# Kernel tuning notes

Measured on AMD Instinct MI355X. Metric: run time of the kernel, lower is better.

The kernel has to match this reference:

```python
import jax, jax.numpy as jnp
import numpy as np

NUM_HEADS = 8
SPARSITY = 0.25
BOUNDARY_W = 0.5
LN_EPS = 1e-5


def setup_inputs() -> dict:
    key = jax.random.key(0)
    ks = jax.random.split(key, 16)
    B, C, H, W = 8, 256, 64, 64
    Ch = C // 4
    s = lambda *sh: 1.0 / np.sqrt(sh[-1])
    inp = {
        'x': jax.random.normal(ks[0], (B, C, H, W), jnp.float32),
        'boundary_map': jax.random.uniform(ks[1], (B, 1, H, W), jnp.float32),
        'imp_w1': jax.random.normal(ks[2], (Ch, C), jnp.float32) * s(C),
        'imp_b1': jnp.zeros((Ch,), jnp.float32),
        'imp_w2': jax.random.normal(ks[3], (1, Ch), jnp.float32) * s(Ch),
        'imp_b2': jnp.zeros((1,), jnp.float32),
        'wq': jax.random.normal(ks[4], (C, C), jnp.float32) * s(C),
        'bq': jnp.zeros((C,), jnp.float32),
        'wk': jax.random.normal(ks[5], (C, C), jnp.float32) * s(C),
        'bk': jnp.zeros((C,), jnp.float32),
        'wv': jax.random.normal(ks[6], (C, C), jnp.float32) * s(C),
        'bv': jnp.zeros((C,), jnp.float32),
        'wo': jax.random.normal(ks[7], (C, C), jnp.float32) * (0.1 * s(C)),
        'bo': jnp.zeros((C,), jnp.float32),
        'ln_g': jnp.ones((C,), jnp.float32),
        'ln_b': jnp.zeros((C,), jnp.float32),
    }
    return inp


def reference(x, boundary_map, imp_w1, imp_b1, imp_w2, imp_b2,
              wq, bq, wk, bk, wv, bv, wo, bo, ln_g, ln_b):
    B, C, H, W = x.shape
    N = H * W
    K = max(int(N * SPARSITY), 1)
    nh = NUM_HEADS
    hd = C // nh
    scale = hd ** -0.5

    # importance net: 1x1 conv -> GELU -> 1x1 conv -> sigmoid
    h = jnp.einsum('bchw,oc->bohw', x, imp_w1) + imp_b1[None, :, None, None]
    h = jax.nn.gelu(h, approximate=False)
    imp = jnp.einsum('bchw,oc->bohw', h, imp_w2) + imp_b2[None, :, None, None]
    importance = jax.nn.sigmoid(imp) + BOUNDARY_W * boundary_map  # [B,1,H,W]

    # top-K token selection
    _, top_idx = jax.lax.top_k(importance.reshape(B, N), K)  # [B,K]

    x_flat = x.transpose(0, 2, 3, 1).reshape(B, N, C)
    x_sp = jnp.take_along_axis(x_flat, top_idx[..., None], axis=1)  # [B,K,C]

    # sparse self-attention over K tokens
    q = (jnp.einsum('bkc,oc->bko', x_sp, wq) + bq).reshape(B, K, nh, hd)
    k = (jnp.einsum('bkc,oc->bko', x_sp, wk) + bk).reshape(B, K, nh, hd)
    v = (jnp.einsum('bkc,oc->bko', x_sp, wv) + bv).reshape(B, K, nh, hd)
    attn = jax.nn.softmax(jnp.einsum('bqhd,bkhd->bhqk', q, k) * scale, axis=-1)
    o = jnp.einsum('bhqk,bkhd->bqhd', attn, v).reshape(B, K, C)
    out_sp = jnp.einsum('bkc,oc->bko', o, wo) + bo

    # residual + LayerNorm
    y = out_sp + x_sp
    mu = jnp.mean(y, axis=-1, keepdims=True)
    var = jnp.mean(jnp.square(y - mu), axis=-1, keepdims=True)
    enh = (y - mu) * jax.lax.rsqrt(var + LN_EPS) * ln_g + ln_b  # [B,K,C]

    # scatter enhanced tokens back
    bidx = jnp.arange(B)[:, None]
    out_full = x_flat.at[bidx, top_idx].set(enh)
    out = out_full.reshape(B, H, W, C).transpose(0, 3, 1, 2)
    return out, importance
```

## Files before the change

### kernel.cpp

```cpp
#include <hip/hip_runtime.h>
#include <math.h>

#define B_ 8
#define C_ 256
#define N_ 4096
#define K_ 1024
#define NH_ 8
#define HD_ 32

typedef __attribute__((ext_vector_type(8))) short short8;
typedef __attribute__((ext_vector_type(8))) _Float16 half8;
typedef __attribute__((ext_vector_type(4))) _Float16 half4;
typedef __attribute__((ext_vector_type(4))) float f32x4;

#if __has_builtin(__builtin_amdgcn_exp2f)
#define EXPX(x) __builtin_amdgcn_exp2f(x)
#define QSCALE (0.17677669529663688f * 1.4426950408889634f)
#else
#define EXPX(x) __expf(x)
#define QSCALE 0.17677669529663688f
#endif

__device__ __forceinline__ unsigned bfr(float x){
  unsigned u = __float_as_uint(x);
  return (u + 0x7FFFu + ((u >> 16) & 1u)) >> 16;
}
__device__ __forceinline__ unsigned pk2(float lo, float hi){
  return bfr(lo) | (bfr(hi) << 16);
}
__device__ __forceinline__ unsigned hpk(float a, float b){
  _Float16 ha = (_Float16)a, hb = (_Float16)b;
  unsigned short ua = __builtin_bit_cast(unsigned short, ha);
  unsigned short ub = __builtin_bit_cast(unsigned short, hb);
  return (unsigned)ua | ((unsigned)ub << 16);
}
__device__ __forceinline__ half4 pk4rtz(float a, float b, float c, float d){
  auto lo = __builtin_amdgcn_cvt_pkrtz(a, b);
  auto hi = __builtin_amdgcn_cvt_pkrtz(c, d);
  uint2 u = make_uint2(__builtin_bit_cast(unsigned, lo), __builtin_bit_cast(unsigned, hi));
  return __builtin_bit_cast(half4, u);
}

__global__ __launch_bounds__(256) void w2h_kernel(
    const float* __restrict__ wq, const float* __restrict__ wk,
    const float* __restrict__ wv, const float* __restrict__ wo,
    unsigned short* __restrict__ wh)
{
  const float* src = blockIdx.y==0 ? wq : blockIdx.y==1 ? wk : blockIdx.y==2 ? wv : wo;
  const int e = (blockIdx.x*256 + threadIdx.x)*8;
  float4 a = *(const float4*)(src + e);
  float4 b = *(const float4*)(src + e + 4);
  uint4 o;
  o.x = hpk(a.x, a.y); o.y = hpk(a.z, a.w);
  o.z = hpk(b.x, b.y); o.w = hpk(b.z, b.w);
  *(uint4*)(wh + (size_t)blockIdx.y*65536 + e) = o;
}

__global__ __launch_bounds__(256) void imp_kernel(
    const float* __restrict__ x, const float* __restrict__ bmap,
    const float* __restrict__ w1, const float* __restrict__ b1,
    const float* __restrict__ w2, const float* __restrict__ b2,
    float* __restrict__ imp_out, float* __restrict__ outx)
{
  __shared__ float xs[256][32];
  __shared__ float red[4][32];
  const int t = threadIdx.x;
  const int b = blockIdx.x >> 7, tile = blockIdx.x & 127;
  const int n0 = tile * 32;
  {
    const int p4 = t & 7, co = t >> 3;
    const float* xb = x + (size_t)b*C_*N_ + n0 + 4*p4;
    float* ox = outx + (size_t)b*C_*N_ + n0 + 4*p4;
    #pragma unroll
    for (int s = 0; s < 8; s++){
      const int c = s*32 + co;
      float4 v = *(const float4*)(xb + (size_t)c*N_);
      *(float4*)(ox + (size_t)c*N_) = v;
      *(float4*)&xs[c][4*(p4 ^ (c & 7))] = v;
    }
  }
  __syncthreads();
  const int pg = t & 7, og = t >> 3;
  float acc[4][2];
  #pragma unroll
  for (int pp=0;pp<4;pp++){ acc[pp][0]=0.f; acc[pp][1]=0.f; }
  #pragma unroll 2
  for (int c8 = 0; c8 < 256; c8 += 8){
    float4 xv[8];
    #pragma unroll
    for (int ci = 0; ci < 8; ci++){
      const int c = c8 + ci;
      xv[ci] = *(const float4*)&xs[c][4*(pg ^ (c & 7))];
    }
    #pragma unroll
    for (int oo = 0; oo < 2; oo++){
      const float* wr = w1 + (size_t)(og + 32*oo)*C_ + c8;
      float4 wa = *(const float4*)wr;
      float4 wb = *(const float4*)(wr+4);
      #pragma unroll
      for (int pp = 0; pp < 4; pp++){
        const float x0 = (&xv[0].x)[pp], x1 = (&xv[1].x)[pp];
        const float x2 = (&xv[2].x)[pp], x3 = (&xv[3].x)[pp];
        const float x4 = (&xv[4].x)[pp], x5 = (&xv[5].x)[pp];
        const float x6 = (&xv[6].x)[pp], x7 = (&xv[7].x)[pp];
        acc[pp][oo] += x0*wa.x + x1*wa.y + x2*wa.z + x3*wa.w
                     + x4*wb.x + x5*wb.y + x6*wb.z + x7*wb.w;
      }
    }
  }
  float part[4] = {0.f,0.f,0.f,0.f};
  #pragma unroll
  for (int oo=0;oo<2;oo++){
    const int o = og + 32*oo;
    const float b1o = b1[o], w2o = w2[o];
    #pragma unroll
    for (int pp=0;pp<4;pp++){
      float a = acc[pp][oo] + b1o;
      float g = 0.5f*a*(1.f + erff(a*0.70710678118654752f));
      part[pp] += w2o*g;
    }
  }
  #pragma unroll
  for (int pp=0;pp<4;pp++){
    part[pp] += __shfl_xor(part[pp], 8);
    part[pp] += __shfl_xor(part[pp], 16);
    part[pp] += __shfl_xor(part[pp], 32);
  }
  const int w = t >> 6;
  if ((t & 63) < 8){
    #pragma unroll
    for (int pp=0;pp<4;pp++) red[w][4*(t&7)+pp] = part[pp];
  }
  __syncthreads();
  if (t < 32){
    float s = red[0][t]+red[1][t]+red[2][t]+red[3][t] + b2[0];
    float sig = 1.f/(1.f+expf(-s));
    imp_out[(size_t)b*N_ + n0 + t] = sig + 0.5f*bmap[(size_t)b*N_ + n0 + t];
  }
}

__global__ __launch_bounds__(1024) void topk_kernel(const float* __restrict__ imp, int* __restrict__ tidx)
{
  __shared__ unsigned long long s[4096];
  __shared__ int ws2[16];
  const int b = blockIdx.x, t = threadIdx.x;
  const float* ib = imp + (size_t)b*N_;
  for (int m = t; m < N_; m += 1024){
    unsigned u = __float_as_uint(ib[m]);
    u = (u & 0x80000000u) ? ~u : (u | 0x80000000u);
    s[m] = ((unsigned long long)u << 32) | (unsigned)(~m);
  }
  for (int k = 2; k <= 4096; k <<= 1){
    for (int j = k >> 1; j > 0; j >>= 1){
      __syncthreads();
      #pragma unroll 2
      for (int m = t; m < 2048; m += 1024){
        int i = 2*m - (m & (j-1));
        int l = i + j;
        unsigned long long a = s[i], c = s[l];
        if ((a > c) == ((i & k) == 0)){ s[i] = c; s[l] = a; }
      }
    }
  }
  __syncthreads();
  const unsigned long long thr = s[3072];
  int sel[4]; int cnt = 0;
  #pragma unroll
  for (int u2 = 0; u2 < 4; u2++){
    const int m = 4*t + u2;
    unsigned u = __float_as_uint(ib[m]);
    u = (u & 0x80000000u) ? ~u : (u | 0x80000000u);
    unsigned long long key = ((unsigned long long)u << 32) | (unsigned)(~m);
    sel[u2] = (key >= thr) ? 1 : 0;
    cnt += sel[u2];
  }
  int incl = cnt;
  #pragma unroll
  for (int d2 = 1; d2 < 64; d2 <<= 1){
    int v2 = __shfl_up(incl, d2);
    if ((t & 63) >= d2) incl += v2;
  }
  if ((t & 63) == 63) ws2[t >> 6] = incl;
  __syncthreads();
  int base = 0;
  const int wv2 = t >> 6;
  #pragma unroll
  for (int ww = 0; ww < 16; ww++) if (ww < wv2) base += ws2[ww];
  int pos = base + incl - cnt;
  #pragma unroll
  for (int u2 = 0; u2 < 4; u2++){
    if (sel[u2]) tidx[(size_t)b*K_ + pos++] = 4*t + u2;
  }
}

__global__ __launch_bounds__(512) void qkv_kernel(
    const float* __restrict__ x, const int* __restrict__ tidx,
    const unsigned short* __restrict__ wh,
    const float* __restrict__ bq, const float* __restrict__ bk, const float* __restrict__ bv,
    float* __restrict__ xsp, unsigned short* __restrict__ qbf,
    unsigned short* __restrict__ kbf, unsigned short* __restrict__ vtb)
{
  __shared__ unsigned short xsb[16][256];
  const int t = threadIdx.x;
  const int kt = blockIdx.x, b = blockIdx.y;
  const int tok0 = kt*16;
  {
    const int i = t & 15, jg = t >> 4;
    const int n = tidx[(size_t)b*K_ + tok0 + i];
    const float* xb = x + (size_t)b*C_*N_ + n;
    float v[8];
    #pragma unroll
    for (int u = 0; u < 8; u++) v[u] = xb[(size_t)(jg*8+u)*N_];
    float* xr = xsp + ((size_t)b*K_ + tok0 + i)*C_ + jg*8;
    *(float4*)(xr)     = make_float4(v[0],v[1],v[2],v[3]);
    *(float4*)(xr + 4) = make_float4(v[4],v[5],v[6],v[7]);
    uint4 pw;
    pw.x = hpk(v[0],v[1]); pw.y = hpk(v[2],v[3]);
    pw.z = hpk(v[4],v[5]); pw.w = hpk(v[6],v[7]);
    *(uint4*)((char*)&xsb[0][0] + i*512 + ((jg ^ (i&7))*16)) = pw;
  }
  __syncthreads();

  const int lane = t & 63, w = t >> 6;
  const int g = lane >> 4, c = lane & 15;

  f32x4 acc[3][2];
  #pragma unroll
  for (int s=0;s<3;s++)
    #pragma unroll
    for (int j=0;j<2;j++) acc[s][j] = (f32x4){0.f,0.f,0.f,0.f};

  #pragma unroll 1
  for (int ks = 0; ks < 8; ks++){
    half8 Xf = *(const half8*)((const char*)&xsb[0][0] + c*512 + (((4*ks+g) ^ (c&7))*16));
    half8 Wf[3][2];
    #pragma unroll
    for (int s=0;s<3;s++)
      #pragma unroll
      for (int j=0;j<2;j++)
        Wf[s][j] = *(const half8*)(wh + (size_t)s*65536 + (32*w + 16*j + c)*C_ + ks*32 + 8*g);
    acc[0][0] = __builtin_amdgcn_mfma_f32_16x16x32_f16(Wf[0][0], Xf, acc[0][0], 0,0,0);
    acc[0][1] = __builtin_amdgcn_mfma_f32_16x16x32_f16(Wf[0][1], Xf, acc[0][1], 0,0,0);
    acc[1][0] = __builtin_amdgcn_mfma_f32_16x16x32_f16(Wf[1][0], Xf, acc[1][0], 0,0,0);
    acc[1][1] = __builtin_amdgcn_mfma_f32_16x16x32_f16(Wf[1][1], Xf, acc[1][1], 0,0,0);
    acc[2][0] = __builtin_amdgcn_mfma_f32_16x16x32_f16(Xf, Wf[2][0], acc[2][0], 0,0,0);
    acc[2][1] = __builtin_amdgcn_mfma_f32_16x16x32_f16(Xf, Wf[2][1], acc[2][1], 0,0,0);
  }

  const int bh = b*NH_ + w;
  #pragma unroll
  for (int s=0;s<2;s++){
    const float* bias = s ? bk : bq;
    const float sc = s ? 1.f : QSCALE;
    unsigned short* dstb = s ? kbf : qbf;
    #pragma unroll
    for (int j=0;j<2;j++){
      f32x4 a = acc[s][j];
      float4 bb = *(const float4*)(bias + w*32 + 16*j + 4*g);
      unsigned lo = pk2((a[0]+bb.x)*sc, (a[1]+bb.y)*sc);
      unsigned hi = pk2((a[2]+bb.z)*sc, (a[3]+bb.w)*sc);
      unsigned short* dst = dstb + ((size_t)bh*K_ + tok0 + c)*HD_ + 16*j + 4*g;
      *(uint2*)dst = make_uint2(lo, hi);
    }
  }
  const int base32 = tok0 & ~31;
  const int half   = (tok0 >> 4) & 1;
  #pragma unroll
  for (int j=0;j<2;j++){
    f32x4 a = acc[2][j];
    const float bvv = bv[w*32 + 16*j + c];
    unsigned lo = hpk(a[0]+bvv, a[1]+bvv);
    unsigned hi = hpk(a[2]+bvv, a[3]+bvv);
    unsigned short* dst = vtb + ((size_t)bh*HD_ + 16*j + c)*K_ + base32 + 8*g + 4*half;
    *(uint2*)dst = make_uint2(lo, hi);
  }
}

__global__ __launch_bounds__(512) void attn_kernel(
    const unsigned short* __restrict__ qbf, const unsigned short* __restrict__ kbf,
    const unsigned short* __restrict__ vtb, unsigned short* __restrict__ ob)
{
  __shared__ float po[4][64][19];
  const int tid = threadIdx.x;
  const int t = tid & 63, w = tid >> 6;
  const int sp = w >> 2, qq = w & 3;
  const int flat = blockIdx.x;
  const int h = flat & 7;
  const int rest = flat >> 3;
  const int qt = rest & 7;
  const int b = rest >> 3;
  const int g = t >> 4, c = t & 15;
  const int bh = b*NH_ + h;
  const int q0 = qt*128 + qq*32;

  short8 Qf0 = *(const short8*)(qbf + ((size_t)bh*K_ + q0 + c)*HD_ + g*8);
  short8 Qf1 = *(const short8*)(qbf + ((size_t)bh*K_ + q0 + 16 + c)*HD_ + g*8);

  const int kbeg = sp*512;
  const unsigned short* kp  = kbf + (size_t)bh*K_*HD_ + (size_t)(kbeg + c)*HD_ + g*8;
  const unsigned short* vp0 = vtb + ((size_t)bh*HD_ + c)*K_ + kbeg + g*8;
  const unsigned short* vp1 = vp0 + (size_t)16*K_;

  const half4 ONES = {(_Float16)1.f, (_Float16)1.f, (_Float16)1.f, (_Float16)1.f};
  f32x4 ot00 = {0.f,0.f,0.f,0.f}, ot01 = {0.f,0.f,0.f,0.f};
  f32x4 ot10 = {0.f,0.f,0.f,0.f}, ot11 = {0.f,0.f,0.f,0.f};
  f32x4 otL0 = {0.f,0.f,0.f,0.f}, otL1 = {0.f,0.f,0.f,0.f};

#define ATTN_STEP(K0c,K1c,V0c,V1c) do {                                           \
    f32x4 z = {0.f,0.f,0.f,0.f};                                                  \
    __builtin_amdgcn_s_setprio(1);                                                \
    f32x4 s00 = __builtin_amdgcn_mfma_f32_16x16x32_bf16(K0c, Qf0, z, 0, 0, 0);    \
    f32x4 s01 = __builtin_amdgcn_mfma_f32_16x16x32_bf16(K1c, Qf0, z, 0, 0, 0);    \
    f32x4 s10 = __builtin_amdgcn_mfma_f32_16x16x32_bf16(K0c, Qf1, z, 0, 0, 0);    \
    f32x4 s11 = __builtin_amdgcn_mfma_f32_16x16x32_bf16(K1c, Qf1, z, 0, 0, 0);    \
    __builtin_amdgcn_s_setprio(0);                                                \
    float p00[4], p01[4], p10[4], p11[4];                                         \
    _Pragma("unroll")                                                             \
    for (int r=0;r<4;r++){                                                        \
      p00[r] = EXPX(s00[r]); p01[r] = EXPX(s01[r]);                               \
      p10[r] = EXPX(s10[r]); p11[r] = EXPX(s11[r]);                               \
    }                                                                             \
    half4 P00 = pk4rtz(p00[0], p00[1], p00[2], p00[3]);                           \
    half4 P01 = pk4rtz(p01[0], p01[1], p01[2], p01[3]);                           \
    half4 P10 = pk4rtz(p10[0], p10[1], p10[2], p10[3]);                           \
    half4 P11 = pk4rtz(p11[0], p11[1], p11[2], p11[3]);                           \
    half4 A0lo = __builtin_shufflevector(V0c, V0c, 0, 1, 2, 3);                   \
    half4 A0hi = __builtin_shufflevector(V0c, V0c, 4, 5, 6, 7);                   \
    half4 A1lo = __builtin_shufflevector(V1c, V1c, 0, 1, 2, 3);                   \
    half4 A1hi = __builtin_shufflevector(V1c, V1c, 4, 5, 6, 7);                   \
    __builtin_amdgcn_s_setprio(1);                                                \
    ot00 = __builtin_amdgcn_mfma_f32_16x16x16f16(A0lo, P00, ot00, 0, 0, 0);       \
    ot00 = __builtin_amdgcn_mfma_f32_16x16x16f16(A0hi, P01, ot00, 0, 0, 0);       \
    ot01 = __builtin_amdgcn_mfma_f32_16x16x16f16(A1lo, P00, ot01, 0, 0, 0);       \
    ot01 = __builtin_amdgcn_mfma_f32_16x16x16f16(A1hi, P01, ot01, 0, 0, 0);       \
    ot10 = __builtin_amdgcn_mfma_f32_16x16x16f16(A0lo, P10, ot10, 0, 0, 0);       \
    ot10 = __builtin_amdgcn_mfma_f32_16x16x16f16(A0hi, P11, ot10, 0, 0, 0);       \
    ot11 = __builtin_amdgcn_mfma_f32_16x16x16f16(A1lo, P10, ot11, 0, 0, 0);       \
    ot11 = __builtin_amdgcn_mfma_f32_16x16x16f16(A1hi, P11, ot11, 0, 0, 0);       \
    otL0 = __builtin_amdgcn_mfma_f32_16x16x16f16(ONES, P00, otL0, 0, 0, 0);       \
    otL0 = __builtin_amdgcn_mfma_f32_16x16x16f16(ONES, P01, otL0, 0, 0, 0);       \
    otL1 = __builtin_amdgcn_mfma_f32_16x16x16f16(ONES, P10, otL1, 0, 0, 0);       \
    otL1 = __builtin_amdgcn_mfma_f32_16x16x16f16(ONES, P11, otL1, 0, 0, 0);       \
    __builtin_amdgcn_s_setprio(0);                                                \
  } while(0)

  short8 K0a = *(const short8*)(kp);
  short8 K1a = *(const short8*)(kp + 16*HD_);
  half8  V0a = *(const half8*)(vp0);
  half8  V1a = *(const half8*)(vp1);
  kp += 32*HD_; vp0 += 32; vp1 += 32;
  short8 K0b = *(const short8*)(kp);
  short8 K1b = *(const short8*)(kp + 16*HD_);
  half8  V0b = *(const half8*)(vp0);
  half8  V1b = *(const half8*)(vp1);

  for (int it = 0; it < 16; it += 2){
    kp += 32*HD_; vp0 += 32; vp1 += 32;
    short8 K0n = *(const short8*)(kp);
    short8 K1n = *(const short8*)(kp + 16*HD_);
    half8  V0n = *(const half8*)(vp0);
    half8  V1n = *(const half8*)(vp1);
    ATTN_STEP(K0a, K1a, V0a, V1a);
    K0a = K0n; K1a = K1n; V0a = V0n; V1a = V1n;
    kp += 32*HD_; vp0 += 32; vp1 += 32;
    short8 K0m = *(const short8*)(kp);
    short8 K1m = *(const short8*)(kp + 16*HD_);
    half8  V0m = *(const half8*)(vp0);
    half8  V1m = *(const half8*)(vp1);
    ATTN_STEP(K0b, K1b, V0b, V1b);
    K0b = K0m; K1b = K1m; V0b = V0m; V1b = V1m;
  }
#undef ATTN_STEP

  if (sp == 1){
    float* d = po[qq][t];
    d[0]=ot00[0]; d[1]=ot00[1]; d[2]=ot00[2];  d[3]=ot00[3];
    d[4]=ot01[0]; d[5]=ot01[1]; d[6]=ot01[2];  d[7]=ot01[3];
    d[8]=ot10[0]; d[9]=ot10[1]; d[10]=ot10[2]; d[11]=ot10[3];
    d[12]=ot11[0];d[13]=ot11[1];d[14]=ot11[2]; d[15]=ot11[3];
    d[16]=otL0[0]; d[17]=otL1[0];
  }
  __syncthreads();
  if (sp == 0){
    const float* d = po[qq][t];
    ot00[0]+=d[0]; ot00[1]+=d[1]; ot00[2]+=d[2];  ot00[3]+=d[3];
    ot01[0]+=d[4]; ot01[1]+=d[5]; ot01[2]+=d[6];  ot01[3]+=d[7];
    ot10[0]+=d[8]; ot10[1]+=d[9]; ot10[2]+=d[10]; ot10[3]+=d[11];
    ot11[0]+=d[12];ot11[1]+=d[13];ot11[2]+=d[14]; ot11[3]+=d[15];
    const float L0 = otL0[0] + d[16];
    const float L1 = otL1[0] + d[17];
    const float i0 = 1.f / L0, i1 = 1.f / L1;
    unsigned short* o0 = ob + ((size_t)b*K_ + q0 + c)*C_ + h*HD_;
    unsigned short* o1 = ob + ((size_t)b*K_ + q0 + 16 + c)*C_ + h*HD_;
    *(uint2*)(o0 + 4*g)      = make_uint2(hpk(ot00[0]*i0, ot00[1]*i0), hpk(ot00[2]*i0, ot00[3]*i0));
    *(uint2*)(o0 + 16 + 4*g) = make_uint2(hpk(ot01[0]*i0, ot01[1]*i0), hpk(ot01[2]*i0, ot01[3]*i0));
    *(uint2*)(o1 + 4*g)      = make_uint2(hpk(ot10[0]*i1, ot10[1]*i1), hpk(ot10[2]*i1, ot10[3]*i1));
    *(uint2*)(o1 + 16 + 4*g) = make_uint2(hpk(ot11[0]*i1, ot11[1]*i1), hpk(ot11[2]*i1, ot11[3]*i1));
  }
}

__global__ __launch_bounds__(512) void out_kernel(
    const unsigned short* __restrict__ ob, const float* __restrict__ xsp,
    const int* __restrict__ tidx, const unsigned short* __restrict__ woh, const float* __restrict__ bo,
    const float* __restrict__ lng, const float* __restrict__ lnb,
    float* __restrict__ out)
{
  __shared__ float red1[8][32], red2[8][32];
  __shared__ float mus[32], rss[32];
  __shared__ int nn[32];
  const int t = threadIdx.x;
  const int kt = blockIdx.x, b = blockIdx.y;
  const int tok0 = kt*32;
  const int lane = t & 63, w = t >> 6;
  const int g = lane >> 4, c = lane & 15;

  if (t < 32) nn[t] = tidx[(size_t)b*K_ + tok0 + t];

  f32x4 acc[2][2];
  #pragma unroll
  for (int j=0;j<2;j++)
    #pragma unroll
    for (int tt=0;tt<2;tt++) acc[j][tt] = (f32x4){0.f,0.f,0.f,0.f};

  const unsigned short* ob0 = ob + ((size_t)b*K_ + tok0)*C_;
  const unsigned short* wr0 = woh + (32*w + c)*C_;

  #pragma unroll 1
  for (int ks = 0; ks < 8; ks++){
    half8 Wf0 = *(const half8*)(wr0 + ks*32 + 8*g);
    half8 Wf1 = *(const half8*)(wr0 + 16*C_ + ks*32 + 8*g);
    #pragma unroll
    for (int tt=0;tt<2;tt++){
      half8 Of = *(const half8*)(ob0 + (size_t)(16*tt + c)*C_ + ks*32 + 8*g);
      acc[0][tt] = __builtin_amdgcn_mfma_f32_16x16x32_f16(Wf0, Of, acc[0][tt], 0,0,0);
      acc[1][tt] = __builtin_amdgcn_mfma_f32_16x16x32_f16(Wf1, Of, acc[1][tt], 0,0,0);
    }
  }

  float4 bb[2];
  #pragma unroll
  for (int j=0;j<2;j++) bb[j] = *(const float4*)(bo + 32*w + 16*j + 4*g);
  #pragma unroll
  for (int tt=0;tt<2;tt++){
    const float* xr = xsp + ((size_t)b*K_ + tok0 + 16*tt + c)*C_ + 32*w + 4*g;
    #pragma unroll
    for (int j=0;j<2;j++){
      float4 xv = *(const float4*)(xr + 16*j);
      acc[j][tt][0] += bb[j].x + xv.x;
      acc[j][tt][1] += bb[j].y + xv.y;
      acc[j][tt][2] += bb[j].z + xv.z;
      acc[j][tt][3] += bb[j].w + xv.w;
    }
  }

  #pragma unroll
  for (int tt=0;tt<2;tt++){
    float s1 = 0.f, s2 = 0.f;
    #pragma unroll
    for (int j=0;j<2;j++)
      #pragma unroll
      for (int r=0;r<4;r++){ float y = acc[j][tt][r]; s1 += y; s2 += y*y; }
    s1 += __shfl_xor(s1, 16); s2 += __shfl_xor(s2, 16);
    s1 += __shfl_xor(s1, 32); s2 += __shfl_xor(s2, 32);
    if (g == 0){ red1[w][16*tt + c] = s1; red2[w][16*tt + c] = s2; }
  }
  __syncthreads();
  if (t < 32){
    float a = 0.f, q2 = 0.f;
    #pragma unroll
    for (int ww=0;ww<8;ww++){ a += red1[ww][t]; q2 += red2[ww][t]; }
    float mu = a*(1.f/256.f);
    float var = q2*(1.f/256.f) - mu*mu;
    mus[t] = mu;
    rss[t] = rsqrtf(var + 1e-5f);
  }
  __syncthreads();

  float4 gv[2], bv2[2];
  #pragma unroll
  for (int j=0;j<2;j++){
    gv[j]  = *(const float4*)(lng + 32*w + 16*j + 4*g);
    bv2[j] = *(const float4*)(lnb + 32*w + 16*j + 4*g);
  }
  float* outb = out + (size_t)b*C_*N_;
  #pragma unroll
  for (int tt=0;tt<2;tt++){
    const int tok = 16*tt + c;
    const float mu = mus[tok], rs = rss[tok];
    const int n = nn[tok];
    #pragma unroll
    for (int j=0;j<2;j++){
      const int oc0 = 32*w + 16*j + 4*g;
      const float* gvp = (const float*)&gv[j];
      const float* bvp = (const float*)&bv2[j];
      #pragma unroll
      for (int r=0;r<4;r++)
        outb[(size_t)(oc0 + r)*N_ + n] = (acc[j][tt][r]-mu)*rs*gvp[r] + bvp[r];
    }
  }
}

extern "C" void kernel_launch(void* const* d_in, const int* in_sizes, int n_in,
                              void* d_out, int out_size, void* d_ws, size_t ws_size,
                              hipStream_t stream)
{
  const float* x    = (const float*)d_in[0];
  const float* bmap = (const float*)d_in[1];
  const float* w1   = (const float*)d_in[2];
  const float* b1   = (const float*)d_in[3];
  const float* w2   = (const float*)d_in[4];
  const float* b2   = (const float*)d_in[5];
  const float* wq   = (const float*)d_in[6];
  const float* bq   = (const float*)d_in[7];
  const float* wk   = (const float*)d_in[8];
  const float* bk   = (const float*)d_in[9];
  const float* wv   = (const float*)d_in[10];
  const float* bv   = (const float*)d_in[11];
  const float* wo   = (const float*)d_in[12];
  const float* bo   = (const float*)d_in[13];
  const float* lng  = (const float*)d_in[14];
  const float* lnb  = (const float*)d_in[15];

  float* out = (float*)d_out;
  float* imp_out = out + (size_t)B_*C_*N_;

  char* wsb = (char*)d_ws;
  int*   tidx = (int*)wsb;
  float* xsp  = (float*)(wsb + 65536);
  unsigned short* ob16 = (unsigned short*)(xsp + (size_t)B_*K_*C_);
  unsigned short* qbf = ob16 + 2*(size_t)B_*K_*C_;
  unsigned short* kbf = qbf + (size_t)B_*NH_*K_*HD_;
  unsigned short* vtb = kbf + (size_t)B_*NH_*K_*HD_;
  unsigned short* wh  = vtb + (size_t)B_*NH_*K_*HD_;

  w2h_kernel <<<dim3(32, 4),    dim3(256),  0, stream>>>(wq, wk, wv, wo, wh);
  imp_kernel <<<dim3(1024),     dim3(256),  0, stream>>>(x, bmap, w1, b1, w2, b2, imp_out, out);
  topk_kernel<<<dim3(8),        dim3(1024), 0, stream>>>(imp_out, tidx);
  qkv_kernel <<<dim3(64, 8),    dim3(512),  0, stream>>>(x, tidx, wh, bq, bk, bv, xsp, qbf, kbf, vtb);
  attn_kernel<<<dim3(512),      dim3(512),  0, stream>>>(qbf, kbf, vtb, ob16);
  out_kernel <<<dim3(32, 8),    dim3(512),  0, stream>>>(ob16, xsp, tidx, wh + 3*65536, bo, lng, lnb, out);
}
```

Measured before the change: 148.5 us.

## Replace full bitonic top-k with radix histogram select, fuse weight conversion

The top-k kernel builds a 4096-bin histogram on the high 12 bits of the importance keys, finds the boundary bin by suffix scan, and bitonic-sorts only the keys in that bin to get the exact threshold. This replaces a full 4096-element sort per batch, which had many barrier-separated stages. The fp32-to-fp16 weight conversion now runs as extra blocks of the top-k launch, removing one kernel launch. The output-projection kernel handles 16 tokens per block instead of 32, doubling the grid to raise parallelism at the cost of reloading the weight fragments more often.

```diff
diff --git a/kernel.cpp b/kernel.cpp
--- a/kernel.cpp
+++ b/kernel.cpp
@@ -39,21 +39,6 @@
   auto hi = __builtin_amdgcn_cvt_pkrtz(c, d);
   uint2 u = make_uint2(__builtin_bit_cast(unsigned, lo), __builtin_bit_cast(unsigned, hi));
   return __builtin_bit_cast(half4, u);
-}
-
-__global__ __launch_bounds__(256) void w2h_kernel(
-    const float* __restrict__ wq, const float* __restrict__ wk,
-    const float* __restrict__ wv, const float* __restrict__ wo,
-    unsigned short* __restrict__ wh)
-{
-  const float* src = blockIdx.y==0 ? wq : blockIdx.y==1 ? wk : blockIdx.y==2 ? wv : wo;
-  const int e = (blockIdx.x*256 + threadIdx.x)*8;
-  float4 a = *(const float4*)(src + e);
-  float4 b = *(const float4*)(src + e + 4);
-  uint4 o;
-  o.x = hpk(a.x, a.y); o.y = hpk(a.z, a.w);
-  o.z = hpk(b.x, b.y); o.w = hpk(b.z, b.w);
-  *(uint4*)(wh + (size_t)blockIdx.y*65536 + e) = o;
 }
 
 __global__ __launch_bounds__(256) void imp_kernel(
@@ -139,54 +124,113 @@
   }
 }
 
-__global__ __launch_bounds__(1024) void topk_kernel(const float* __restrict__ imp, int* __restrict__ tidx)
+__global__ __launch_bounds__(1024) void topk_kernel(
+    const float* __restrict__ imp, int* __restrict__ tidx,
+    const float* __restrict__ wq, const float* __restrict__ wk,
+    const float* __restrict__ wv, const float* __restrict__ wo,
+    unsigned short* __restrict__ wh)
 {
-  __shared__ unsigned long long s[4096];
-  __shared__ int ws2[16];
-  const int b = blockIdx.x, t = threadIdx.x;
+  const int t = threadIdx.x;
+  if (blockIdx.x >= 8){
+    const int idx = blockIdx.x - 8;
+    const int set = idx >> 3, chunk = idx & 7;
+    const float* src = set==0 ? wq : set==1 ? wk : set==2 ? wv : wo;
+    const int e = (chunk*1024 + t)*8;
+    float4 a = *(const float4*)(src + e);
+    float4 b = *(const float4*)(src + e + 4);
+    uint4 o;
+    o.x = hpk(a.x, a.y); o.y = hpk(a.z, a.w);
+    o.z = hpk(b.x, b.y); o.w = hpk(b.z, b.w);
+    *(uint4*)(wh + (size_t)set*65536 + e) = o;
+    return;
+  }
+  __shared__ unsigned hist[4096];
+  __shared__ unsigned long long lst[4096];
+  __shared__ unsigned wsum[16];
+  __shared__ int scal[4];
+  const int b = blockIdx.x;
   const float* ib = imp + (size_t)b*N_;
-  for (int m = t; m < N_; m += 1024){
-    unsigned u = __float_as_uint(ib[m]);
-    u = (u & 0x80000000u) ? ~u : (u | 0x80000000u);
-    s[m] = ((unsigned long long)u << 32) | (unsigned)(~m);
-  }
-  for (int k = 2; k <= 4096; k <<= 1){
+  const int lane = t & 63, w = t >> 6;
+
+  unsigned uu[4];
+  #pragma unroll
+  for (int u2 = 0; u2 < 4; u2++){
+    unsigned u = __float_as_uint(ib[4*t + u2]);
+    uu[u2] = (u & 0x80000000u) ? ~u : (u | 0x80000000u);
+  }
+  hist[t] = 0; hist[t+1024] = 0; hist[t+2048] = 0; hist[t+3072] = 0;
+  if (t == 0) scal[0] = 0;
+  __syncthreads();
+  #pragma unroll
+  for (int u2 = 0; u2 < 4; u2++) atomicAdd(&hist[uu[u2] >> 20], 1u);
+  __syncthreads();
+  const unsigned h0 = hist[4*t], h1 = hist[4*t+1], h2 = hist[4*t+2], h3 = hist[4*t+3];
+  const unsigned s4 = h0 + h1 + h2 + h3;
+  unsigned sfx = s4;
+  #pragma unroll
+  for (int d = 1; d < 64; d <<= 1){
+    unsigned v = __shfl_down(sfx, d);
+    if (lane + d < 64) sfx += v;
+  }
+  if (lane == 0) wsum[w] = sfx;
+  __syncthreads();
+  unsigned Wt = 0;
+  #pragma unroll
+  for (int ww = 0; ww < 16; ww++) if (ww > w) Wt += wsum[ww];
+  const unsigned G3 = Wt + (sfx - s4);
+  const unsigned G2 = G3 + h3, G1 = G2 + h2, G0 = G1 + h1;
+  if (G0 < 1024u && G0 + h0 >= 1024u){ scal[1] = 4*t+0; scal[2] = 1024 - (int)G0; }
+  if (G1 < 1024u && G1 + h1 >= 1024u){ scal[1] = 4*t+1; scal[2] = 1024 - (int)G1; }
+  if (G2 < 1024u && G2 + h2 >= 1024u){ scal[1] = 4*t+2; scal[2] = 1024 - (int)G2; }
+  if (G3 < 1024u && G3 + h3 >= 1024u){ scal[1] = 4*t+3; scal[2] = 1024 - (int)G3; }
+  __syncthreads();
+  const unsigned p = (unsigned)scal[1];
+  const int r = scal[2];
+  #pragma unroll
+  for (int u2 = 0; u2 < 4; u2++){
+    if ((uu[u2] >> 20) == p){
+      int pos = atomicAdd(&scal[0], 1);
+      lst[pos] = ((unsigned long long)uu[u2] << 32) | (unsigned)(~(4*t + u2));
+    }
+  }
+  __syncthreads();
+  const int cnt = scal[0];
+  int pad = 1; while (pad < cnt) pad <<= 1;
+  for (int m = t; m < pad; m += 1024) if (m >= cnt) lst[m] = 0ull;
+  __syncthreads();
+  for (int k = 2; k <= pad; k <<= 1){
     for (int j = k >> 1; j > 0; j >>= 1){
-      __syncthreads();
-      #pragma unroll 2
-      for (int m = t; m < 2048; m += 1024){
+      for (int m = t; m < (pad >> 1); m += 1024){
         int i = 2*m - (m & (j-1));
         int l = i + j;
-        unsigned long long a = s[i], c = s[l];
-        if ((a > c) == ((i & k) == 0)){ s[i] = c; s[l] = a; }
+        unsigned long long a = lst[i], c = lst[l];
+        if ((a > c) == ((i & k) == 0)){ lst[i] = c; lst[l] = a; }
       }
-    }
-  }
-  __syncthreads();
-  const unsigned long long thr = s[3072];
-  int sel[4]; int cnt = 0;
+      __syncthreads();
+    }
+  }
+  const unsigned long long thr = lst[pad - r];
+  __shared__ int ws2[16];
+  int sel[4]; int cnt2 = 0;
   #pragma unroll
   for (int u2 = 0; u2 < 4; u2++){
     const int m = 4*t + u2;
-    unsigned u = __float_as_uint(ib[m]);
-    u = (u & 0x80000000u) ? ~u : (u | 0x80000000u);
-    unsigned long long key = ((unsigned long long)u << 32) | (unsigned)(~m);
+    unsigned long long key = ((unsigned long long)uu[u2] << 32) | (unsigned)(~m);
     sel[u2] = (key >= thr) ? 1 : 0;
-    cnt += sel[u2];
-  }
-  int incl = cnt;
+    cnt2 += sel[u2];
+  }
+  int incl = cnt2;
   #pragma unroll
   for (int d2 = 1; d2 < 64; d2 <<= 1){
     int v2 = __shfl_up(incl, d2);
-    if ((t & 63) >= d2) incl += v2;
-  }
-  if ((t & 63) == 63) ws2[t >> 6] = incl;
+    if (lane >= d2) incl += v2;
+  }
+  if (lane == 63) ws2[w] = incl;
   __syncthreads();
   int base = 0;
-  const int wv2 = t >> 6;
-  #pragma unroll
-  for (int ww = 0; ww < 16; ww++) if (ww < wv2) base += ws2[ww];
-  int pos = base + incl - cnt;
+  #pragma unroll
+  for (int ww = 0; ww < 16; ww++) if (ww < w) base += ws2[ww];
+  int pos = base + incl - cnt2;
   #pragma unroll
   for (int u2 = 0; u2 < 4; u2++){
     if (sel[u2]) tidx[(size_t)b*K_ + pos++] = 4*t + u2;
@@ -405,22 +449,18 @@
     const float* __restrict__ lng, const float* __restrict__ lnb,
     float* __restrict__ out)
 {
-  __shared__ float red1[8][32], red2[8][32];
-  __shared__ float mus[32], rss[32];
-  __shared__ int nn[32];
+  __shared__ float red1[8][16], red2[8][16];
+  __shared__ float mus[16], rss[16];
+  __shared__ int nn[16];
   const int t = threadIdx.x;
   const int kt = blockIdx.x, b = blockIdx.y;
-  const int tok0 = kt*32;
+  const int tok0 = kt*16;
   const int lane = t & 63, w = t >> 6;
   const int g = lane >> 4, c = lane & 15;
 
-  if (t < 32) nn[t] = tidx[(size_t)b*K_ + tok0 + t];
-
-  f32x4 acc[2][2];
-  #pragma unroll
-  for (int j=0;j<2;j++)
-    #pragma unroll
-    for (int tt=0;tt<2;tt++) acc[j][tt] = (f32x4){0.f,0.f,0.f,0.f};
+  if (t < 16) nn[t] = tidx[(size_t)b*K_ + tok0 + t];
+
+  f32x4 acc0 = {0.f,0.f,0.f,0.f}, acc1 = {0.f,0.f,0.f,0.f};
 
   const unsigned short* ob0 = ob + ((size_t)b*K_ + tok0)*C_;
   const unsigned short* wr0 = woh + (32*w + c)*C_;
@@ -429,43 +469,35 @@
   for (int ks = 0; ks < 8; ks++){
     half8 Wf0 = *(const half8*)(wr0 + ks*32 + 8*g);
     half8 Wf1 = *(const half8*)(wr0 + 16*C_ + ks*32 + 8*g);
-    #pragma unroll
-    for (int tt=0;tt<2;tt++){
-      half8 Of = *(const half8*)(ob0 + (size_t)(16*tt + c)*C_ + ks*32 + 8*g);
-      acc[0][tt] = __builtin_amdgcn_mfma_f32_16x16x32_f16(Wf0, Of, acc[0][tt], 0,0,0);
-      acc[1][tt] = __builtin_amdgcn_mfma_f32_16x16x32_f16(Wf1, Of, acc[1][tt], 0,0,0);
-    }
-  }
-
-  float4 bb[2];
-  #pragma unroll
-  for (int j=0;j<2;j++) bb[j] = *(const float4*)(bo + 32*w + 16*j + 4*g);
-  #pragma unroll
-  for (int tt=0;tt<2;tt++){
-    const float* xr = xsp + ((size_t)b*K_ + tok0 + 16*tt + c)*C_ + 32*w + 4*g;
-    #pragma unroll
-    for (int j=0;j<2;j++){
-      float4 xv = *(const float4*)(xr + 16*j);
-      acc[j][tt][0] += bb[j].x + xv.x;
-      acc[j][tt][1] += bb[j].y + xv.y;
-      acc[j][tt][2] += bb[j].z + xv.z;
-      acc[j][tt][3] += bb[j].w + xv.w;
-    }
-  }
-
-  #pragma unroll
-  for (int tt=0;tt<2;tt++){
+    half8 Of  = *(const half8*)(ob0 + (size_t)c*C_ + ks*32 + 8*g);
+    acc0 = __builtin_amdgcn_mfma_f32_16x16x32_f16(Wf0, Of, acc0, 0,0,0);
+    acc1 = __builtin_amdgcn_mfma_f32_16x16x32_f16(Wf1, Of, acc1, 0,0,0);
+  }
+
+  const float* xr = xsp + ((size_t)b*K_ + tok0 + c)*C_ + 32*w + 4*g;
+  {
+    float4 bb0 = *(const float4*)(bo + 32*w + 4*g);
+    float4 bb1 = *(const float4*)(bo + 32*w + 16 + 4*g);
+    float4 xv0 = *(const float4*)(xr);
+    float4 xv1 = *(const float4*)(xr + 16);
+    acc0[0] += bb0.x + xv0.x; acc0[1] += bb0.y + xv0.y;
+    acc0[2] += bb0.z + xv0.z; acc0[3] += bb0.w + xv0.w;
+    acc1[0] += bb1.x + xv1.x; acc1[1] += bb1.y + xv1.y;
+    acc1[2] += bb1.z + xv1.z; acc1[3] += bb1.w + xv1.w;
+  }
+
+  {
     float s1 = 0.f, s2 = 0.f;
     #pragma unroll
-    for (int j=0;j<2;j++)
-      #pragma unroll
-      for (int r=0;r<4;r++){ float y = acc[j][tt][r]; s1 += y; s2 += y*y; }
+    for (int r=0;r<4;r++){ float y = acc0[r]; s1 += y; s2 += y*y; }
+    #pragma unroll
+    for (int r=0;r<4;r++){ float y = acc1[r]; s1 += y; s2 += y*y; }
     s1 += __shfl_xor(s1, 16); s2 += __shfl_xor(s2, 16);
     s1 += __shfl_xor(s1, 32); s2 += __shfl_xor(s2, 32);
-    if (g == 0){ red1[w][16*tt + c] = s1; red2[w][16*tt + c] = s2; }
-  }
-  __syncthreads();
-  if (t < 32){
+    if (g == 0){ red1[w][c] = s1; red2[w][c] = s2; }
+  }
+  __syncthreads();
+  if (t < 16){
     float a = 0.f, q2 = 0.f;
     #pragma unroll
     for (int ww=0;ww<8;ww++){ a += red1[ww][t]; q2 += red2[ww][t]; }
@@ -476,27 +508,19 @@
   }
   __syncthreads();
 
-  float4 gv[2], bv2[2];
+  const float mu = mus[c], rs = rss[c];
+  const int n = nn[c];
+  float* outb = out + (size_t)b*C_*N_;
   #pragma unroll
   for (int j=0;j<2;j++){
-    gv[j]  = *(const float4*)(lng + 32*w + 16*j + 4*g);
-    bv2[j] = *(const float4*)(lnb + 32*w + 16*j + 4*g);
-  }
-  float* outb = out + (size_t)b*C_*N_;
-  #pragma unroll
-  for (int tt=0;tt<2;tt++){
-    const int tok = 16*tt + c;
-    const float mu = mus[tok], rs = rss[tok];
-    const int n = nn[tok];
-    #pragma unroll
-    for (int j=0;j<2;j++){
-      const int oc0 = 32*w + 16*j + 4*g;
-      const float* gvp = (const float*)&gv[j];
-      const float* bvp = (const float*)&bv2[j];
-      #pragma unroll
-      for (int r=0;r<4;r++)
-        outb[(size_t)(oc0 + r)*N_ + n] = (acc[j][tt][r]-mu)*rs*gvp[r] + bvp[r];
-    }
+    const int oc0 = 32*w + 16*j + 4*g;
+    float4 gvv = *(const float4*)(lng + oc0);
+    float4 bvv = *(const float4*)(lnb + oc0);
+    const f32x4& a = j ? acc1 : acc0;
+    outb[(size_t)(oc0+0)*N_ + n] = (a[0]-mu)*rs*gvv.x + bvv.x;
+    outb[(size_t)(oc0+1)*N_ + n] = (a[1]-mu)*rs*gvv.y + bvv.y;
+    outb[(size_t)(oc0+2)*N_ + n] = (a[2]-mu)*rs*gvv.z + bvv.z;
+    outb[(size_t)(oc0+3)*N_ + n] = (a[3]-mu)*rs*gvv.w + bvv.w;
   }
 }
 
@@ -533,10 +557,9 @@
   unsigned short* vtb = kbf + (size_t)B_*NH_*K_*HD_;
   unsigned short* wh  = vtb + (size_t)B_*NH_*K_*HD_;
 
-  w2h_kernel <<<dim3(32, 4),    dim3(256),  0, stream>>>(wq, wk, wv, wo, wh);
   imp_kernel <<<dim3(1024),     dim3(256),  0, stream>>>(x, bmap, w1, b1, w2, b2, imp_out, out);
-  topk_kernel<<<dim3(8),        dim3(1024), 0, stream>>>(imp_out, tidx);
+  topk_kernel<<<dim3(40),       dim3(1024), 0, stream>>>(imp_out, tidx, wq, wk, wv, wo, wh);
   qkv_kernel <<<dim3(64, 8),    dim3(512),  0, stream>>>(x, tidx, wh, bq, bk, bv, xsp, qbf, kbf, vtb);
   attn_kernel<<<dim3(512),      dim3(512),  0, stream>>>(qbf, kbf, vtb, ob16);
-  out_kernel <<<dim3(32, 8),    dim3(512),  0, stream>>>(ob16, xsp, tidx, wh + 3*65536, bo, lng, lnb, out);
-}
+  out_kernel <<<dim3(64, 8),    dim3(512),  0, stream>>>(ob16, xsp, tidx, wh + 3*65536, bo, lng, lnb, out);
+}
```

After: 129.3 us. -12.9%, faster.
